# Kernel optimization log

Measured on AMD Instinct MI355X. Metric: run time of the kernel, lower is better.

The kernel has to match this reference:

```python
import jax, jax.numpy as jnp
import numpy as np

TOP_K = 8
RECENCY_DECAY = 0.99
CURRENT_TS = 1.0


def _normalize(x, eps=1e-12):
    # matches torch F.normalize: x / max(||x||_2, eps)
    n = jnp.linalg.norm(x, axis=-1, keepdims=True)
    return x / jnp.maximum(n, eps)


def setup_inputs() -> dict:
    key = jax.random.key(0)
    ks = jax.random.split(key, 7)
    B, N, H = 2048, 65536, 1024
    return {
        "query": jax.random.normal(ks[0], (B, H), dtype=jnp.float32),
        "store": jax.random.normal(ks[1], (N, H), dtype=jnp.float32),
        "importance": jax.random.uniform(ks[2], (N,), dtype=jnp.float32),
        "timestamps": jax.random.uniform(ks[3], (N,), dtype=jnp.float32),
        "Wk": jax.random.normal(ks[4], (H, H), dtype=jnp.float32) / np.sqrt(H),
        "Wv": jax.random.normal(ks[5], (H, H), dtype=jnp.float32) / np.sqrt(H),
        "Wo": jax.random.normal(ks[6], (H, H), dtype=jnp.float32) / np.sqrt(H),
    }


def reference(query, store, importance, timestamps, Wk, Wv, Wo):
    # key/value projections over the full store (Linear, no bias)
    keys = store @ Wk.T          # [N, H]
    vals = store @ Wv.T          # [N, H]

    # recency/importance weighting
    ages = CURRENT_TS - timestamps
    recency = jnp.exp(-jnp.abs(ages) * (1.0 - RECENCY_DECAY))
    weights = recency * (importance + 1.0)
    weights = weights / (weights.sum() + 1e-8)  # [N]

    # cosine similarity scaled by weights
    q_norm = _normalize(query)   # [B, H]
    k_norm = _normalize(keys)    # [N, H]
    sim = (q_norm @ k_norm.T) * weights[None, :]  # [B, N]

    # top-k retrieval + softmax-weighted combine
    topk_sim, topk_idx = jax.lax.top_k(sim, TOP_K)   # [B, k]
    attn = jax.nn.softmax(topk_sim, axis=-1)          # [B, k]
    topk_vals = vals[topk_idx]                        # [B, k, H]
    out = jnp.einsum("bk,bkh->bh", attn, topk_vals)  # [B, H]
    return out @ Wo.T
```

## Files before the change

### kernel.cpp

```cpp
#include <hip/hip_runtime.h>
#include <stdint.h>

typedef _Float16 f16;
typedef _Float16 f16x8 __attribute__((ext_vector_type(8)));
typedef _Float16 f16x4 __attribute__((ext_vector_type(4)));
typedef float    f32x4 __attribute__((ext_vector_type(4)));

#define B_DIM 2048
#define N_DIM 65536
#define H_DIM 1024

__device__ __forceinline__ unsigned short f32_to_bf16(float f) {
    unsigned int u = __builtin_bit_cast(unsigned int, f);
    unsigned int r = u + 0x7fffu + ((u >> 16) & 1u);
    return (unsigned short)(r >> 16);
}

typedef const __attribute__((address_space(1))) void g_void;
typedef __attribute__((address_space(3))) void l_void;
__device__ __forceinline__ void glds16(const void* g, void* l) {
    __builtin_amdgcn_global_load_lds((g_void*)g, (l_void*)l, 16, 0, 0);
}

__global__ __launch_bounds__(256) void k_weights(const float* __restrict__ imp,
                                                 const float* __restrict__ ts,
                                                 float* __restrict__ w,
                                                 float* __restrict__ sumw) {
    int i = blockIdx.x * 256 + threadIdx.x;
    float age = 1.0f - ts[i];
    float r = expf(-fabsf(age) * (float)(1.0 - 0.99));
    float wv = r * (imp[i] + 1.0f);
    w[i] = wv;
    for (int off = 32; off; off >>= 1) wv += __shfl_down(wv, off, 64);
    __shared__ float ps[4];
    if ((threadIdx.x & 63) == 0) ps[threadIdx.x >> 6] = wv;
    __syncthreads();
    if (threadIdx.x == 0) atomicAdd(sumw, ps[0] + ps[1] + ps[2] + ps[3]);
}

__global__ __launch_bounds__(256) void k_split(const float* __restrict__ x,
                                               f16* __restrict__ hi, f16* __restrict__ lo) {
    size_t i = (size_t)blockIdx.x * 256 + threadIdx.x;
    float4 v0 = ((const float4*)x)[2 * i];
    float4 v1 = ((const float4*)x)[2 * i + 1];
    float vv[8] = {v0.x, v0.y, v0.z, v0.w, v1.x, v1.y, v1.z, v1.w};
    f16x8 h, l;
#pragma unroll
    for (int j = 0; j < 8; j++) { h[j] = (f16)vv[j]; l[j] = (f16)(vv[j] - (float)h[j]); }
    ((f16x8*)hi)[i] = h;
    ((f16x8*)lo)[i] = l;
}

__global__ __launch_bounds__(256) void k_tohalf(const float* __restrict__ x, f16* __restrict__ h) {
    size_t i = (size_t)blockIdx.x * 256 + threadIdx.x;
    float4 v0 = ((const float4*)x)[2 * i];
    float4 v1 = ((const float4*)x)[2 * i + 1];
    f16x8 o = {(f16)v0.x, (f16)v0.y, (f16)v0.z, (f16)v0.w,
               (f16)v1.x, (f16)v1.y, (f16)v1.z, (f16)v1.w};
    ((f16x8*)h)[i] = o;
}

__global__ __launch_bounds__(256) void k_qnorm(const float* __restrict__ q,
                                               float* __restrict__ qn, f16* __restrict__ q16) {
    int b = blockIdx.x, t = threadIdx.x;
    float4 v = ((const float4*)(q + (size_t)b * H_DIM))[t];
    float ss = v.x * v.x + v.y * v.y + v.z * v.z + v.w * v.w;
    for (int off = 32; off; off >>= 1) ss += __shfl_down(ss, off, 64);
    __shared__ float ps[4];
    if ((t & 63) == 0) ps[t >> 6] = ss;
    __syncthreads();
    float tot = ps[0] + ps[1] + ps[2] + ps[3];
    float rn = 1.0f / fmaxf(sqrtf(tot), 1e-12f);
    float4 o;
    o.x = v.x * rn; o.y = v.y * rn; o.z = v.z * rn; o.w = v.w * rn;
    ((float4*)(qn + (size_t)b * H_DIM))[t] = o;
    f16x4 h = {(f16)o.x, (f16)o.y, (f16)o.z, (f16)o.w};
    ((f16x4*)(q16 + (size_t)b * H_DIM))[t] = h;
}

__global__ __launch_bounds__(256) void k_rowstats(const float* __restrict__ keys,
                                                  const float* __restrict__ w,
                                                  const float* __restrict__ sumw,
                                                  float* __restrict__ sscale) {
    int n = blockIdx.x, t = threadIdx.x;
    float4 v = ((const float4*)(keys + (size_t)n * H_DIM))[t];
    float ss = v.x * v.x + v.y * v.y + v.z * v.z + v.w * v.w;
    for (int off = 32; off; off >>= 1) ss += __shfl_down(ss, off, 64);
    __shared__ float ps[4];
    if ((t & 63) == 0) ps[t >> 6] = ss;
    __syncthreads();
    if (t == 0) {
        float tot = ps[0] + ps[1] + ps[2] + ps[3];
        sscale[n] = w[n] / ((sumw[0] + 1e-8f) * fmaxf(sqrtf(tot), 1e-12f));
    }
}


#define RD_A(AB, H)                                                              \
    _Pragma("unroll") for (int mi = 0; mi < 4; ++mi) {                           \
        a[mi][0] = *(const f16x8*)(lds + (AB) + arow + (H)*8192 + mi*2048 + acol0); \
        a[mi][1] = *(const f16x8*)(lds + (AB) + arow + (H)*8192 + mi*2048 + acol1); \
    }

#define RD_B(DST, BB, OFFH)                                                      \
    _Pragma("unroll") for (int nj = 0; nj < 2; ++nj) {                           \
        DST[nj][0] = *(const f16x8*)(lds + (BB) + (OFFH) + brow + nj*2048 + acol0); \
        DST[nj][1] = *(const f16x8*)(lds + (BB) + (OFFH) + brow + nj*2048 + acol1); \
    }

#define PH_PRE()                                                                 \
    __builtin_amdgcn_s_barrier();                                                \
    asm volatile("s_waitcnt lgkmcnt(0)" ::: "memory");                           \
    __builtin_amdgcn_sched_barrier(0);                                           \
    __builtin_amdgcn_s_setprio(1);

#define PH_POST()                                                                \
    __builtin_amdgcn_s_setprio(0);                                               \
    __builtin_amdgcn_s_barrier();

#define MFMA8x2(MH, BV, NB)                                                      \
    _Pragma("unroll") for (int ks = 0; ks < 2; ++ks)                             \
    _Pragma("unroll") for (int mi = 0; mi < 4; ++mi)                             \
    _Pragma("unroll") for (int nj = 0; nj < 2; ++nj)                             \
        acc[(MH)*4 + mi][(NB) + nj] = __builtin_amdgcn_mfma_f32_16x16x32_f16(    \
            a[mi][ks], BV[nj][ks], acc[(MH)*4 + mi][(NB) + nj], 0, 0, 0);

#define TILE_BODY(T, STG, W0STR)                                                 \
  {                                                                              \
    const int cur = (T) & 1;                                                     \
    const int ab = cur * 32768;                                                  \
    const int bb = 65536 + cur * 32768;                                          \
    const int da = (cur ^ 1) * 32768;                                            \
    const int db = 65536 + (cur ^ 1) * 32768;                                    \
    const f16* An = A0; const f16* Bn = Bh; int toffn = 0;                       \
    if (STG) {                                                                   \
        const int tn = (T) + 1;                                                  \
        if constexpr (OUTMODE == 0) {                                            \
            An = (tn < 16) ? A0 : (tn < 32 ? A1 : A0);                           \
            Bn = (tn < 32) ? Bh : Bl;                                            \
            toffn = (tn & 15) * 64;                                             \
        } else { toffn = tn * 64; }                                             \
    }                                                                            \
                                                    \
    RD_A(ab, 0)                                                                  \
    RD_B(b0, bb, 0)                                                              \
    if (STG) {                                                                   \
        glds16(An + aoff0 + toffn, lds + da + tid * 16);                         \
        glds16(An + aoff2 + toffn, lds + da + 16384 + tid * 16);                 \
        glds16(Bn + boffE1 + toffn, lds + db + tid * 16);                        \
        glds16(Bn + boffE2 + toffn, lds + db + 8192 + tid * 16);                 \
    }                                                                            \
    asm volatile("s_waitcnt vmcnt(" W0STR ")" ::: "memory");                     \
    PH_PRE() MFMA8x2(0, b0, 0) PH_POST()                                         \
                                                     \
    RD_B(b1, bb, 16384)                                                          \
    if (STG) {                                                                   \
        glds16(Bn + boffO1 + toffn, lds + db + 16384 + tid * 16);                \
        glds16(Bn + boffO2 + toffn, lds + db + 24576 + tid * 16);                \
        glds16(An + aoff1 + toffn, lds + da + 8192 + tid * 16);                  \
        glds16(An + aoff3 + toffn, lds + da + 24576 + tid * 16);                 \
    }                                                                            \
    PH_PRE() MFMA8x2(0, b1, 2) PH_POST()                                         \
                                                     \
    RD_A(ab, 1)                                                                  \
    PH_PRE() MFMA8x2(1, b1, 2) PH_POST()                                         \
                                                    \
    asm volatile("s_waitcnt vmcnt(4)" ::: "memory");                             \
    PH_PRE() MFMA8x2(1, b0, 0) PH_POST()                                         \
  }

template <int OUTMODE>
__global__ __launch_bounds__(512) void k_gemm8(
    const f16* __restrict__ A0, const f16* __restrict__ A1,
    const f16* __restrict__ Bh, const f16* __restrict__ Bl,
    float* __restrict__ of32, f16* __restrict__ of16,
    unsigned short* __restrict__ obf16, const float* __restrict__ colscale) {
    __shared__ char lds[131072];
    const int tid = threadIdx.x;

    constexpr int NT = (OUTMODE == 0) ? 48 : 16;
    constexpr int Cs = (OUTMODE == 0) ? H_DIM : N_DIM;

    int m0, n0;
    {
        const int f = blockIdx.x;
        if constexpr (OUTMODE == 0) {
            const int lg = (f & 7) * 128 + (f >> 3);
            m0 = (lg >> 2) * 256; n0 = (lg & 3) * 256;
        } else {
            const int lg = (f & 7) * 256 + (f >> 3);
            m0 = (lg & 7) * 256; n0 = (lg >> 3) * 256;
        }
    }

    const int sr = tid >> 3, ss = tid & 7;
    const int ssw = (ss ^ (sr & 7)) * 8;
    const size_t aoff0 = (size_t)(m0 + sr) * H_DIM + ssw;
    const size_t aoff1 = (size_t)(m0 + 64 + sr) * H_DIM + ssw;
    const size_t aoff2 = (size_t)(m0 + 128 + sr) * H_DIM + ssw;
    const size_t aoff3 = (size_t)(m0 + 192 + sr) * H_DIM + ssw;
    const int nE = (sr >> 5) * 64 + (sr & 31);
    const size_t boffE1 = (size_t)(n0 + nE) * H_DIM + ssw;
    const size_t boffE2 = (size_t)(n0 + nE + 128) * H_DIM + ssw;
    const size_t boffO1 = (size_t)(n0 + nE + 32) * H_DIM + ssw;
    const size_t boffO2 = (size_t)(n0 + nE + 160) * H_DIM + ssw;

    const int lane = tid & 63, wave = tid >> 6;
    const int wr = wave >> 2, wc = wave & 3;
    const int m16 = lane & 15, q4 = lane >> 4;
    const int axor = (lane & 7) << 4;
    const int acol0 = (q4 * 16) ^ axor;
    const int acol1 = (64 + q4 * 16) ^ axor;
    const int arow = (wr * 128 + m16) * 128;
    const int brow = (wc * 32 + m16) * 128;

    f32x4 acc[8][4];
#pragma unroll
    for (int i = 0; i < 8; i++)
#pragma unroll
        for (int j = 0; j < 4; j++) acc[i][j] = (f32x4){0.f, 0.f, 0.f, 0.f};
    f16x8 a[4][2], b0[2][2], b1[2][2];

    glds16(A0 + aoff0, lds + tid * 16);
    glds16(A0 + aoff2, lds + 16384 + tid * 16);
    glds16(Bh + boffE1, lds + 65536 + tid * 16);
    glds16(Bh + boffE2, lds + 65536 + 8192 + tid * 16);
    glds16(Bh + boffO1, lds + 65536 + 16384 + tid * 16);
    glds16(Bh + boffO2, lds + 65536 + 24576 + tid * 16);
    glds16(A0 + aoff1, lds + 8192 + tid * 16);
    glds16(A0 + aoff3, lds + 24576 + tid * 16);
    asm volatile("s_waitcnt vmcnt(4)" ::: "memory");
    __builtin_amdgcn_s_barrier();

    for (int t = 0; t < NT - 1; ++t) TILE_BODY(t, 1, "4")
    TILE_BODY(NT - 1, 0, "0")

    float cs0 = 0.f, cs1 = 0.f, cs2 = 0.f, cs3 = 0.f;
    if constexpr (OUTMODE == 1) {
        cs0 = colscale[n0 + wc * 64 + m16];
        cs1 = colscale[n0 + wc * 64 + 16 + m16];
        cs2 = colscale[n0 + wc * 64 + 32 + m16];
        cs3 = colscale[n0 + wc * 64 + 48 + m16];
    }
#pragma unroll
    for (int mi = 0; mi < 8; ++mi) {
        const int rowb = m0 + wr * 128 + mi * 16 + q4 * 4;
#pragma unroll
        for (int njj = 0; njj < 4; ++njj) {
            const int col = n0 + wc * 64 + (njj >> 1) * 32 + (njj & 1) * 16 + m16;
            const float c = (njj == 0) ? cs0 : (njj == 1) ? cs1 : (njj == 2) ? cs2 : cs3;
#pragma unroll
            for (int rr = 0; rr < 4; ++rr) {
                const float v = acc[mi][njj][rr];
                const size_t o = (size_t)(rowb + rr) * Cs + col;
                if constexpr (OUTMODE == 0) { of32[o] = v; of16[o] = (f16)v; }
                else obf16[o] = f32_to_bf16(v * c);
            }
        }
    }
    (void)A1; (void)Bl; (void)colscale;
}

template <int OUTMODE>
__global__ __launch_bounds__(256) void k_gemm64(const f16* __restrict__ A, const f16* __restrict__ B,
                                                float* __restrict__ of32, f16* __restrict__ of16) {
    __shared__ f16 As[64 * 32];
    __shared__ f16 Bs[128 * 32];
    const int tid = threadIdx.x;
    const int m0 = blockIdx.y * 64, n0 = blockIdx.x * 128;
    const int r = tid >> 2, c8 = (tid & 3) * 8;
    const f16* ga = A + (size_t)(m0 + r) * H_DIM + c8;
    const f16* gb0 = B + (size_t)(n0 + r) * H_DIM + c8;
    const f16* gb1 = B + (size_t)(n0 + r + 64) * H_DIM + c8;

    const int lane = tid & 63, wave = tid >> 6;
    const int wn = wave * 32;
    const int q4 = lane >> 4, m16 = lane & 15;
    const int aoff = m16 * 32 + q4 * 8;
    const int boff = (wn + m16) * 32 + q4 * 8;

    f32x4 acc[4][2];
#pragma unroll
    for (int i = 0; i < 4; i++)
#pragma unroll
        for (int j = 0; j < 2; j++) acc[i][j] = (f32x4){0.f, 0.f, 0.f, 0.f};

    for (int k0 = 0; k0 < H_DIM; k0 += 32) {
        __syncthreads();
        glds16(ga + k0, As + tid * 8);
        glds16(gb0 + k0, Bs + tid * 8);
        glds16(gb1 + k0, Bs + 2048 + tid * 8);
        __syncthreads();
        f16x8 a[4], b[2];
#pragma unroll
        for (int i = 0; i < 4; i++) a[i] = *(const f16x8*)(As + aoff + i * 512);
#pragma unroll
        for (int j = 0; j < 2; j++) b[j] = *(const f16x8*)(Bs + boff + j * 512);
#pragma unroll
        for (int i = 0; i < 4; i++)
#pragma unroll
            for (int j = 0; j < 2; j++)
                acc[i][j] = __builtin_amdgcn_mfma_f32_16x16x32_f16(a[i], b[j], acc[i][j], 0, 0, 0);
    }

#pragma unroll
    for (int i = 0; i < 4; i++) {
        const int rowb = m0 + i * 16 + q4 * 4;
#pragma unroll
        for (int j = 0; j < 2; j++) {
            const int col = n0 + wn + j * 16 + m16;
#pragma unroll
            for (int rr = 0; rr < 4; rr++) {
                const float v = acc[i][j][rr];
                const size_t o = (size_t)(rowb + rr) * H_DIM + col;
                if constexpr (OUTMODE == 2) of16[o] = (f16)v;
                else of32[o] = v;
            }
        }
    }
}

__global__ __launch_bounds__(256) void k_chunk_top8(const unsigned short* __restrict__ sim,
                                                    unsigned int* __restrict__ ck) {
    const int ch = blockIdx.x, b = blockIdx.y, t = threadIdx.x;
    const unsigned short* p = sim + (size_t)b * N_DIM + (size_t)ch * 4096 + t * 16;
    uint4 d0 = ((const uint4*)p)[0];
    uint4 d1 = ((const uint4*)p)[1];
    unsigned int raw[8] = {d0.x, d0.y, d0.z, d0.w, d1.x, d1.y, d1.z, d1.w};
    unsigned int key[16];
#pragma unroll
    for (int i = 0; i < 8; i++) {
        unsigned int lo16 = raw[i] & 0xFFFFu, hi16 = raw[i] >> 16;
        lo16 ^= (lo16 & 0x8000u) ? 0xFFFFu : 0x8000u;
        hi16 ^= (hi16 & 0x8000u) ? 0xFFFFu : 0x8000u;
        key[2 * i]     = (lo16 << 16) | (unsigned)(t * 16 + 2 * i);
        key[2 * i + 1] = (hi16 << 16) | (unsigned)(t * 16 + 2 * i + 1);
    }
    unsigned int lm = 0;
#pragma unroll
    for (int i = 0; i < 16; i++) lm = max(lm, key[i]);

    __shared__ unsigned int wmax[2][4];
    const int w = t >> 6;
    unsigned int* outp = ck + (size_t)(b * 16 + ch) * 8;
    for (int rnd = 0; rnd < 8; ++rnd) {
        unsigned int u = lm;
        for (int off = 32; off; off >>= 1) u = max(u, __shfl_down(u, off, 64));
        if ((t & 63) == 0) wmax[rnd & 1][w] = u;
        __syncthreads();
        unsigned int win = max(max(wmax[rnd & 1][0], wmax[rnd & 1][1]),
                               max(wmax[rnd & 1][2], wmax[rnd & 1][3]));
        if (t == 0) outp[rnd] = win;
        if (((win & 0xFFFu) >> 4) == (unsigned)t) {
            key[win & 15u] = 0;
            lm = 0;
#pragma unroll
            for (int i = 0; i < 16; i++) lm = max(lm, key[i]);
        }
    }
}

__global__ __launch_bounds__(256) void k_merge(const unsigned int* __restrict__ ck,
                                               const float* __restrict__ qn,
                                               const float* __restrict__ keys32,
                                               const float* __restrict__ sscale,
                                               const float* __restrict__ store,
                                               f16* __restrict__ s16) {
    const int b = blockIdx.x, t = threadIdx.x;
    __shared__ unsigned int cks[128];
    __shared__ unsigned int wmax2[2][2];
    __shared__ int c16[16];
    __shared__ float rs[16];
    __shared__ float a8[8];
    __shared__ int i8[8];

    if (t < 128) cks[t] = ck[(size_t)b * 128 + t];
    __syncthreads();
    unsigned int r2 = (t < 128) ? ((cks[t] & 0xFFFF0000u) | (unsigned)t) : 0u;

    for (int rnd = 0; rnd < 16; ++rnd) {
        unsigned int u = r2;
        for (int off = 32; off; off >>= 1) u = max(u, __shfl_down(u, off, 64));
        if ((t & 63) == 0 && t < 128) wmax2[rnd & 1][t >> 6] = u;
        __syncthreads();
        unsigned int win = max(wmax2[rnd & 1][0], wmax2[rnd & 1][1]);
        int j = (int)(win & 127u);
        if (t == 0) c16[rnd] = (j >> 3) * 4096 + (int)(cks[j] & 0xFFFu);
        if (t == j) r2 = 0;
    }
    __syncthreads();

    const int g = t >> 4, l16 = t & 15;
    const int idx = c16[g];
    const float* kr = keys32 + (size_t)idx * H_DIM;
    const float* qr = qn + (size_t)b * H_DIM;
    float sum = 0.f;
#pragma unroll 8
    for (int j = 0; j < 64; j++) {
        int k = l16 + j * 16;
        sum += qr[k] * kr[k];
    }
    for (int off = 8; off; off >>= 1) sum += __shfl_down(sum, off, 16);
    if (l16 == 0) rs[g] = sum * sscale[idx];
    __syncthreads();

    if (t == 0) {
        float v[16];
        for (int i = 0; i < 16; i++) v[i] = rs[i];
        float av[8]; int ai[8];
        for (int it = 0; it < 8; ++it) {
            float bm = -1e30f; int mi = 0;
            for (int i = 0; i < 16; i++)
                if (v[i] > bm) { bm = v[i]; mi = i; }
            av[it] = bm; ai[it] = c16[mi]; v[mi] = -1e30f;
        }
        float m = av[0], e[8], ssum = 0.f;
        for (int k = 0; k < 8; k++) { e[k] = expf(av[k] - m); ssum += e[k]; }
        for (int k = 0; k < 8; k++) { a8[k] = e[k] / ssum; i8[k] = ai[k]; }
    }
    __syncthreads();

#pragma unroll
    for (int p = 0; p < 4; p++) {
        const int col = t + p * 256;
        float sum2 = 0.f;
#pragma unroll
        for (int k = 0; k < 8; k++) sum2 += a8[k] * store[(size_t)i8[k] * H_DIM + col];
        s16[(size_t)b * H_DIM + col] = (f16)sum2;
    }
}

#define MB (1024ull * 1024ull)
#define OFF_STOREHI (0ull)
#define OFF_STORELO (128ull * MB)
#define OFF_KEYS32  (256ull * MB)
#define OFF_KEYS16  (512ull * MB)
#define OFF_WKHI    (640ull * MB)
#define OFF_WKLO    (642ull * MB)
#define OFF_WV16    (644ull * MB)
#define OFF_WO16    (646ull * MB)
#define OFF_QN      (648ull * MB)
#define OFF_Q16     (656ull * MB)
#define OFF_W       (660ull * MB)
#define OFF_SSCALE  (660ull * MB + 256ull * 1024ull)
#define OFF_SUMW    (660ull * MB + 512ull * 1024ull)
#define OFF_CK      (661ull * MB)
#define OFF_S16     (664ull * MB)
#define OFF_T16     (668ull * MB)

extern "C" void kernel_launch(void* const* d_in, const int* in_sizes, int n_in,
                              void* d_out, int out_size, void* d_ws, size_t ws_size,
                              hipStream_t stream) {
    const float* q     = (const float*)d_in[0];
    const float* store = (const float*)d_in[1];
    const float* imp   = (const float*)d_in[2];
    const float* ts    = (const float*)d_in[3];
    const float* Wk    = (const float*)d_in[4];
    const float* Wv    = (const float*)d_in[5];
    const float* Wo    = (const float*)d_in[6];
    float* out = (float*)d_out;
    char* ws = (char*)d_ws;

    f16* storeHi = (f16*)(ws + OFF_STOREHI);
    f16* storeLo = (f16*)(ws + OFF_STORELO);
    float* keys32 = (float*)(ws + OFF_KEYS32);
    f16* keys16 = (f16*)(ws + OFF_KEYS16);
    f16* wkHi = (f16*)(ws + OFF_WKHI);
    f16* wkLo = (f16*)(ws + OFF_WKLO);
    f16* wv16 = (f16*)(ws + OFF_WV16);
    f16* wo16 = (f16*)(ws + OFF_WO16);
    float* qn = (float*)(ws + OFF_QN);
    f16* q16 = (f16*)(ws + OFF_Q16);
    float* wbuf = (float*)(ws + OFF_W);
    float* sscale = (float*)(ws + OFF_SSCALE);
    float* sumw = (float*)(ws + OFF_SUMW);
    unsigned int* ck = (unsigned int*)(ws + OFF_CK);
    f16* s16 = (f16*)(ws + OFF_S16);
    f16* t16 = (f16*)(ws + OFF_T16);
    unsigned short* sim = (unsigned short*)(ws + OFF_STOREHI);

    hipMemsetAsync(sumw, 0, 4, stream);

    k_weights<<<N_DIM / 256, 256, 0, stream>>>(imp, ts, wbuf, sumw);
    k_split<<<(N_DIM * H_DIM) / 2048, 256, 0, stream>>>(store, storeHi, storeLo);
    k_split<<<(H_DIM * H_DIM) / 2048, 256, 0, stream>>>(Wk, wkHi, wkLo);
    k_tohalf<<<(H_DIM * H_DIM) / 2048, 256, 0, stream>>>(Wv, wv16);
    k_tohalf<<<(H_DIM * H_DIM) / 2048, 256, 0, stream>>>(Wo, wo16);
    k_qnorm<<<B_DIM, 256, 0, stream>>>(q, qn, q16);

    k_gemm8<0><<<1024, 512, 0, stream>>>(storeHi, storeLo, wkHi, wkLo,
                                         keys32, keys16, nullptr, nullptr);

    k_rowstats<<<N_DIM, 256, 0, stream>>>(keys32, wbuf, sumw, sscale);

    k_gemm8<1><<<2048, 512, 0, stream>>>(q16, nullptr, keys16, nullptr,
                                         nullptr, nullptr, sim, sscale);

    k_chunk_top8<<<dim3(16, B_DIM), 256, 0, stream>>>(sim, ck);
    k_merge<<<B_DIM, 256, 0, stream>>>(ck, qn, keys32, sscale, store, s16);

    k_gemm64<2><<<dim3(H_DIM / 128, B_DIM / 64), 256, 0, stream>>>(s16, wv16, nullptr, t16);
    k_gemm64<3><<<dim3(H_DIM / 128, B_DIM / 64), 256, 0, stream>>>(t16, wo16, out, nullptr);

    (void)in_sizes; (void)n_in; (void)out_size; (void)ws_size;
}
```

Before: 1.342 ms.

## Fold Wk into query side and compute key norms inside projection GEMM

Rewrites q·(store Wk^T)^T as (q Wk)·store^T: the query is projected through Wk with a split-precision small GEMM, and the similarity GEMM then reads the fp16 store directly, so the N×H keys matrix is never materialized. The key projection GEMM now only reduces squared row norms with shuffles and atomics instead of writing fp32 and fp16 keys, and the separate rowstats pass becomes a tiny elementwise finalize. This removes a large amount of global memory traffic, in exchange for an extra transpose-split kernel, atomic contention, and different rounding in the similarity, since fp16 store is used instead of fp16 keys.

```diff
diff --git a/kernel.cpp b/kernel.cpp
--- a/kernel.cpp
+++ b/kernel.cpp
@@ -60,8 +60,31 @@
     ((f16x8*)h)[i] = o;
 }
 
+__global__ __launch_bounds__(256) void k_tsplit(const float* __restrict__ Wm,
+                                                f16* __restrict__ th, f16* __restrict__ tl_) {
+    __shared__ float tl[64][65];
+    const int t = threadIdx.x;
+    const int r0 = blockIdx.y * 64, c0 = blockIdx.x * 64;
+#pragma unroll
+    for (int p = 0; p < 16; ++p) {
+        int idx = p * 256 + t;
+        int r = idx >> 6, c = idx & 63;
+        tl[r][c] = Wm[(size_t)(r0 + r) * H_DIM + c0 + c];
+    }
+    __syncthreads();
+#pragma unroll
+    for (int p = 0; p < 16; ++p) {
+        int idx = p * 256 + t;
+        int oc = idx >> 6, rr = idx & 63;
+        float v = tl[rr][oc];
+        f16 h = (f16)v;
+        th[(size_t)(c0 + oc) * H_DIM + r0 + rr] = h;
+        tl_[(size_t)(c0 + oc) * H_DIM + r0 + rr] = (f16)(v - (float)h);
+    }
+}
+
 __global__ __launch_bounds__(256) void k_qnorm(const float* __restrict__ q,
-                                               float* __restrict__ qn, f16* __restrict__ q16) {
+                                               f16* __restrict__ qh, f16* __restrict__ ql) {
     int b = blockIdx.x, t = threadIdx.x;
     float4 v = ((const float4*)(q + (size_t)b * H_DIM))[t];
     float ss = v.x * v.x + v.y * v.y + v.z * v.z + v.w * v.w;
@@ -71,28 +94,20 @@
     __syncthreads();
     float tot = ps[0] + ps[1] + ps[2] + ps[3];
     float rn = 1.0f / fmaxf(sqrtf(tot), 1e-12f);
-    float4 o;
-    o.x = v.x * rn; o.y = v.y * rn; o.z = v.z * rn; o.w = v.w * rn;
-    ((float4*)(qn + (size_t)b * H_DIM))[t] = o;
-    f16x4 h = {(f16)o.x, (f16)o.y, (f16)o.z, (f16)o.w};
-    ((f16x4*)(q16 + (size_t)b * H_DIM))[t] = h;
-}
-
-__global__ __launch_bounds__(256) void k_rowstats(const float* __restrict__ keys,
-                                                  const float* __restrict__ w,
-                                                  const float* __restrict__ sumw,
-                                                  float* __restrict__ sscale) {
-    int n = blockIdx.x, t = threadIdx.x;
-    float4 v = ((const float4*)(keys + (size_t)n * H_DIM))[t];
-    float ss = v.x * v.x + v.y * v.y + v.z * v.z + v.w * v.w;
-    for (int off = 32; off; off >>= 1) ss += __shfl_down(ss, off, 64);
-    __shared__ float ps[4];
-    if ((t & 63) == 0) ps[t >> 6] = ss;
-    __syncthreads();
-    if (t == 0) {
-        float tot = ps[0] + ps[1] + ps[2] + ps[3];
-        sscale[n] = w[n] / ((sumw[0] + 1e-8f) * fmaxf(sqrtf(tot), 1e-12f));
-    }
+    float o[4] = {v.x * rn, v.y * rn, v.z * rn, v.w * rn};
+    f16x4 h, l;
+#pragma unroll
+    for (int j = 0; j < 4; j++) { h[j] = (f16)o[j]; l[j] = (f16)(o[j] - (float)h[j]); }
+    ((f16x4*)(qh + (size_t)b * H_DIM))[t] = h;
+    ((f16x4*)(ql + (size_t)b * H_DIM))[t] = l;
+}
+
+__global__ __launch_bounds__(256) void k_fin(const float* __restrict__ w,
+                                             const float* __restrict__ sumw,
+                                             const float* __restrict__ nrm2,
+                                             float* __restrict__ sscale) {
+    int i = blockIdx.x * 256 + threadIdx.x;
+    sscale[i] = w[i] / ((sumw[0] + 1e-8f) * fmaxf(sqrtf(nrm2[i]), 1e-12f));
 }
 
 
@@ -138,8 +153,8 @@
         if constexpr (OUTMODE == 0) {                                            \
             An = (tn < 16) ? A0 : (tn < 32 ? A1 : A0);                           \
             Bn = (tn < 32) ? Bh : Bl;                                            \
-            toffn = (tn & 15) * 64;                                             \
-        } else { toffn = tn * 64; }                                             \
+            toffn = (tn & 15) * 64;                                              \
+        } else { toffn = tn * 64; }                                              \
     }                                                                            \
                                                     \
     RD_A(ab, 0)                                                                  \
@@ -173,13 +188,13 @@
 __global__ __launch_bounds__(512) void k_gemm8(
     const f16* __restrict__ A0, const f16* __restrict__ A1,
     const f16* __restrict__ Bh, const f16* __restrict__ Bl,
-    float* __restrict__ of32, f16* __restrict__ of16,
-    unsigned short* __restrict__ obf16, const float* __restrict__ colscale) {
+    unsigned short* __restrict__ obf16, const float* __restrict__ colscale,
+    float* __restrict__ nrm2) {
     __shared__ char lds[131072];
     const int tid = threadIdx.x;
 
     constexpr int NT = (OUTMODE == 0) ? 48 : 16;
-    constexpr int Cs = (OUTMODE == 0) ? H_DIM : N_DIM;
+    constexpr int Cs = N_DIM;
 
     int m0, n0;
     {
@@ -235,43 +250,68 @@
     for (int t = 0; t < NT - 1; ++t) TILE_BODY(t, 1, "4")
     TILE_BODY(NT - 1, 0, "0")
 
-    float cs0 = 0.f, cs1 = 0.f, cs2 = 0.f, cs3 = 0.f;
-    if constexpr (OUTMODE == 1) {
-        cs0 = colscale[n0 + wc * 64 + m16];
-        cs1 = colscale[n0 + wc * 64 + 16 + m16];
-        cs2 = colscale[n0 + wc * 64 + 32 + m16];
-        cs3 = colscale[n0 + wc * 64 + 48 + m16];
-    }
-#pragma unroll
-    for (int mi = 0; mi < 8; ++mi) {
-        const int rowb = m0 + wr * 128 + mi * 16 + q4 * 4;
-#pragma unroll
-        for (int njj = 0; njj < 4; ++njj) {
-            const int col = n0 + wc * 64 + (njj >> 1) * 32 + (njj & 1) * 16 + m16;
-            const float c = (njj == 0) ? cs0 : (njj == 1) ? cs1 : (njj == 2) ? cs2 : cs3;
+    if constexpr (OUTMODE == 0) {
+#pragma unroll
+        for (int mi = 0; mi < 8; ++mi)
 #pragma unroll
             for (int rr = 0; rr < 4; ++rr) {
-                const float v = acc[mi][njj][rr];
-                const size_t o = (size_t)(rowb + rr) * Cs + col;
-                if constexpr (OUTMODE == 0) { of32[o] = v; of16[o] = (f16)v; }
-                else obf16[o] = f32_to_bf16(v * c);
+                float s = 0.f;
+#pragma unroll
+                for (int njj = 0; njj < 4; ++njj) {
+                    float v = acc[mi][njj][rr];
+                    s += v * v;
+                }
+                s += __shfl_xor(s, 1, 64);
+                s += __shfl_xor(s, 2, 64);
+                s += __shfl_xor(s, 4, 64);
+                s += __shfl_xor(s, 8, 64);
+                if (m16 == 0)
+                    atomicAdd(&nrm2[m0 + wr * 128 + mi * 16 + q4 * 4 + rr], s);
             }
-        }
-    }
-    (void)A1; (void)Bl; (void)colscale;
+    } else {
+        float cs0 = colscale[n0 + wc * 64 + m16];
+        float cs1 = colscale[n0 + wc * 64 + 16 + m16];
+        float cs2 = colscale[n0 + wc * 64 + 32 + m16];
+        float cs3 = colscale[n0 + wc * 64 + 48 + m16];
+#pragma unroll
+        for (int mi = 0; mi < 8; ++mi) {
+            const int rowb = m0 + wr * 128 + mi * 16 + q4 * 4;
+#pragma unroll
+            for (int njj = 0; njj < 4; ++njj) {
+                const int col = n0 + wc * 64 + (njj >> 1) * 32 + (njj & 1) * 16 + m16;
+                const float c = (njj == 0) ? cs0 : (njj == 1) ? cs1 : (njj == 2) ? cs2 : cs3;
+#pragma unroll
+                for (int rr = 0; rr < 4; ++rr) {
+                    const float v = acc[mi][njj][rr];
+                    const size_t o = (size_t)(rowb + rr) * Cs + col;
+                    obf16[o] = f32_to_bf16(v * c);
+                }
+            }
+        }
+    }
+    (void)A1; (void)Bl; (void)nrm2; (void)colscale; (void)obf16;
 }
 
 template <int OUTMODE>
-__global__ __launch_bounds__(256) void k_gemm64(const f16* __restrict__ A, const f16* __restrict__ B,
+__global__ __launch_bounds__(256) void k_gemm64(const f16* __restrict__ A, const f16* __restrict__ Al,
+                                                const f16* __restrict__ B, const f16* __restrict__ Bl,
                                                 float* __restrict__ of32, f16* __restrict__ of16) {
     __shared__ f16 As[64 * 32];
     __shared__ f16 Bs[128 * 32];
+    __shared__ f16 AsL[(OUTMODE == 4) ? 64 * 32 : 1];
+    __shared__ f16 BsL[(OUTMODE == 4) ? 128 * 32 : 1];
     const int tid = threadIdx.x;
     const int m0 = blockIdx.y * 64, n0 = blockIdx.x * 128;
     const int r = tid >> 2, c8 = (tid & 3) * 8;
     const f16* ga = A + (size_t)(m0 + r) * H_DIM + c8;
     const f16* gb0 = B + (size_t)(n0 + r) * H_DIM + c8;
     const f16* gb1 = B + (size_t)(n0 + r + 64) * H_DIM + c8;
+    const f16 *gal = nullptr, *gbl0 = nullptr, *gbl1 = nullptr;
+    if constexpr (OUTMODE == 4) {
+        gal = Al + (size_t)(m0 + r) * H_DIM + c8;
+        gbl0 = Bl + (size_t)(n0 + r) * H_DIM + c8;
+        gbl1 = Bl + (size_t)(n0 + r + 64) * H_DIM + c8;
+    }
 
     const int lane = tid & 63, wave = tid >> 6;
     const int wn = wave * 32;
@@ -290,17 +330,33 @@
         glds16(ga + k0, As + tid * 8);
         glds16(gb0 + k0, Bs + tid * 8);
         glds16(gb1 + k0, Bs + 2048 + tid * 8);
+        if constexpr (OUTMODE == 4) {
+            glds16(gal + k0, AsL + tid * 8);
+            glds16(gbl0 + k0, BsL + tid * 8);
+            glds16(gbl1 + k0, BsL + 2048 + tid * 8);
+        }
         __syncthreads();
-        f16x8 a[4], b[2];
+        f16x8 a[4], b[2], al[4], bl[2];
 #pragma unroll
         for (int i = 0; i < 4; i++) a[i] = *(const f16x8*)(As + aoff + i * 512);
 #pragma unroll
         for (int j = 0; j < 2; j++) b[j] = *(const f16x8*)(Bs + boff + j * 512);
+        if constexpr (OUTMODE == 4) {
+#pragma unroll
+            for (int i = 0; i < 4; i++) al[i] = *(const f16x8*)(AsL + aoff + i * 512);
+#pragma unroll
+            for (int j = 0; j < 2; j++) bl[j] = *(const f16x8*)(BsL + boff + j * 512);
+        }
 #pragma unroll
         for (int i = 0; i < 4; i++)
 #pragma unroll
-            for (int j = 0; j < 2; j++)
+            for (int j = 0; j < 2; j++) {
+                if constexpr (OUTMODE == 4) {
+                    acc[i][j] = __builtin_amdgcn_mfma_f32_16x16x32_f16(al[i], b[j], acc[i][j], 0, 0, 0);
+                    acc[i][j] = __builtin_amdgcn_mfma_f32_16x16x32_f16(a[i], bl[j], acc[i][j], 0, 0, 0);
+                }
                 acc[i][j] = __builtin_amdgcn_mfma_f32_16x16x32_f16(a[i], b[j], acc[i][j], 0, 0, 0);
+            }
     }
 
 #pragma unroll
@@ -314,7 +370,8 @@
                 const float v = acc[i][j][rr];
                 const size_t o = (size_t)(rowb + rr) * H_DIM + col;
                 if constexpr (OUTMODE == 2) of16[o] = (f16)v;
-                else of32[o] = v;
+                else if constexpr (OUTMODE == 3) of32[o] = v;
+                else { of32[o] = v; of16[o] = (f16)v; }
             }
         }
     }
@@ -361,8 +418,7 @@
 }
 
 __global__ __launch_bounds__(256) void k_merge(const unsigned int* __restrict__ ck,
-                                               const float* __restrict__ qn,
-                                               const float* __restrict__ keys32,
+                                               const float* __restrict__ qk32,
                                                const float* __restrict__ sscale,
                                                const float* __restrict__ store,
                                                f16* __restrict__ s16) {
@@ -392,8 +448,8 @@
 
     const int g = t >> 4, l16 = t & 15;
     const int idx = c16[g];
-    const float* kr = keys32 + (size_t)idx * H_DIM;
-    const float* qr = qn + (size_t)b * H_DIM;
+    const float* kr = store + (size_t)idx * H_DIM;
+    const float* qr = qk32 + (size_t)b * H_DIM;
     float sum = 0.f;
 #pragma unroll 8
     for (int j = 0; j < 64; j++) {
@@ -433,20 +489,24 @@
 #define MB (1024ull * 1024ull)
 #define OFF_STOREHI (0ull)
 #define OFF_STORELO (128ull * MB)
-#define OFF_KEYS32  (256ull * MB)
-#define OFF_KEYS16  (512ull * MB)
-#define OFF_WKHI    (640ull * MB)
-#define OFF_WKLO    (642ull * MB)
-#define OFF_WV16    (644ull * MB)
-#define OFF_WO16    (646ull * MB)
-#define OFF_QN      (648ull * MB)
-#define OFF_Q16     (656ull * MB)
-#define OFF_W       (660ull * MB)
-#define OFF_SSCALE  (660ull * MB + 256ull * 1024ull)
-#define OFF_SUMW    (660ull * MB + 512ull * 1024ull)
-#define OFF_CK      (661ull * MB)
-#define OFF_S16     (664ull * MB)
-#define OFF_T16     (668ull * MB)
+#define OFF_SIM     (256ull * MB)
+#define OFF_WKHI    (512ull * MB)
+#define OFF_WKLO    (514ull * MB)
+#define OFF_WKTH    (516ull * MB)
+#define OFF_WKTL    (518ull * MB)
+#define OFF_QNHI    (520ull * MB)
+#define OFF_QNLO    (524ull * MB)
+#define OFF_QK32    (528ull * MB)
+#define OFF_QK16    (536ull * MB)
+#define OFF_WV16    (540ull * MB)
+#define OFF_WO16    (542ull * MB)
+#define OFF_W       (544ull * MB)
+#define OFF_SSCALE  (544ull * MB + 256ull * 1024ull)
+#define OFF_SUMW    (544ull * MB + 512ull * 1024ull)
+#define OFF_NRM2    (544ull * MB + 768ull * 1024ull)
+#define OFF_CK      (545ull * MB)
+#define OFF_S16     (546ull * MB)
+#define OFF_T16     (550ull * MB)
 
 extern "C" void kernel_launch(void* const* d_in, const int* in_sizes, int n_in,
                               void* d_out, int out_size, void* d_ws, size_t ws_size,
@@ -463,44 +523,50 @@
 
     f16* storeHi = (f16*)(ws + OFF_STOREHI);
     f16* storeLo = (f16*)(ws + OFF_STORELO);
-    float* keys32 = (float*)(ws + OFF_KEYS32);
-    f16* keys16 = (f16*)(ws + OFF_KEYS16);
+    unsigned short* sim = (unsigned short*)(ws + OFF_SIM);
     f16* wkHi = (f16*)(ws + OFF_WKHI);
     f16* wkLo = (f16*)(ws + OFF_WKLO);
+    f16* wkTh = (f16*)(ws + OFF_WKTH);
+    f16* wkTl = (f16*)(ws + OFF_WKTL);
+    f16* qnHi = (f16*)(ws + OFF_QNHI);
+    f16* qnLo = (f16*)(ws + OFF_QNLO);
+    float* qk32 = (float*)(ws + OFF_QK32);
+    f16* qk16 = (f16*)(ws + OFF_QK16);
     f16* wv16 = (f16*)(ws + OFF_WV16);
     f16* wo16 = (f16*)(ws + OFF_WO16);
-    float* qn = (float*)(ws + OFF_QN);
-    f16* q16 = (f16*)(ws + OFF_Q16);
     float* wbuf = (float*)(ws + OFF_W);
     float* sscale = (float*)(ws + OFF_SSCALE);
     float* sumw = (float*)(ws + OFF_SUMW);
+    float* nrm2 = (float*)(ws + OFF_NRM2);
     unsigned int* ck = (unsigned int*)(ws + OFF_CK);
     f16* s16 = (f16*)(ws + OFF_S16);
     f16* t16 = (f16*)(ws + OFF_T16);
-    unsigned short* sim = (unsigned short*)(ws + OFF_STOREHI);
 
     hipMemsetAsync(sumw, 0, 4, stream);
+    hipMemsetAsync(nrm2, 0, N_DIM * 4, stream);
 
     k_weights<<<N_DIM / 256, 256, 0, stream>>>(imp, ts, wbuf, sumw);
     k_split<<<(N_DIM * H_DIM) / 2048, 256, 0, stream>>>(store, storeHi, storeLo);
     k_split<<<(H_DIM * H_DIM) / 2048, 256, 0, stream>>>(Wk, wkHi, wkLo);
+    k_tsplit<<<dim3(16, 16), 256, 0, stream>>>(Wk, wkTh, wkTl);
     k_tohalf<<<(H_DIM * H_DIM) / 2048, 256, 0, stream>>>(Wv, wv16);
     k_tohalf<<<(H_DIM * H_DIM) / 2048, 256, 0, stream>>>(Wo, wo16);
-    k_qnorm<<<B_DIM, 256, 0, stream>>>(q, qn, q16);
-
-    k_gemm8<0><<<1024, 512, 0, stream>>>(storeHi, storeLo, wkHi, wkLo,
-                                         keys32, keys16, nullptr, nullptr);
-
-    k_rowstats<<<N_DIM, 256, 0, stream>>>(keys32, wbuf, sumw, sscale);
-
-    k_gemm8<1><<<2048, 512, 0, stream>>>(q16, nullptr, keys16, nullptr,
-                                         nullptr, nullptr, sim, sscale);
+    k_qnorm<<<B_DIM, 256, 0, stream>>>(q, qnHi, qnLo);
+
+    k_gemm64<4><<<dim3(H_DIM / 128, B_DIM / 64), 256, 0, stream>>>(
+        qnHi, qnLo, wkTh, wkTl, qk32, qk16);
+
+    k_gemm8<0><<<1024, 512, 0, stream>>>(storeHi, storeLo, wkHi, wkLo, nullptr, nullptr, nrm2);
+
+    k_fin<<<N_DIM / 256, 256, 0, stream>>>(wbuf, sumw, nrm2, sscale);
+
+    k_gemm8<1><<<2048, 512, 0, stream>>>(qk16, nullptr, storeHi, nullptr, sim, sscale, nullptr);
 
     k_chunk_top8<<<dim3(16, B_DIM), 256, 0, stream>>>(sim, ck);
-    k_merge<<<B_DIM, 256, 0, stream>>>(ck, qn, keys32, sscale, store, s16);
-
-    k_gemm64<2><<<dim3(H_DIM / 128, B_DIM / 64), 256, 0, stream>>>(s16, wv16, nullptr, t16);
-    k_gemm64<3><<<dim3(H_DIM / 128, B_DIM / 64), 256, 0, stream>>>(t16, wo16, out, nullptr);
+    k_merge<<<B_DIM, 256, 0, stream>>>(ck, qk32, sscale, store, s16);
+
+    k_gemm64<2><<<dim3(H_DIM / 128, B_DIM / 64), 256, 0, stream>>>(s16, nullptr, wv16, nullptr, nullptr, t16);
+    k_gemm64<3><<<dim3(H_DIM / 128, B_DIM / 64), 256, 0, stream>>>(t16, nullptr, wo16, nullptr, out, nullptr);
 
     (void)in_sizes; (void)n_in; (void)out_size; (void)ws_size;
 }
```

Result: faster. 1.309 ms (-2.4%).
